# Optimization experiments

Hardware: AMD Instinct MI355X
Metric: run time of the kernel (lower is better)

## Reference

```python
import jax, jax.numpy as jnp
import numpy as np


def setup_inputs() -> dict:
    key = jax.random.key(0)
    ks = jax.random.split(key, 5)
    B, T, D, E = 4, 2048, 1024, 8
    inputs = jax.random.normal(ks[0], (B, T, D), dtype=jnp.float32)
    Wr = jax.random.normal(ks[1], (D, E), dtype=jnp.float32) * 0.02
    br = jnp.zeros((E,), dtype=jnp.float32)
    W1 = jax.random.normal(ks[2], (E, D, D), dtype=jnp.float32) * 0.02
    b1 = jnp.zeros((E, D), dtype=jnp.float32)
    W2 = jax.random.normal(ks[3], (E, D, D), dtype=jnp.float32) * 0.02
    b2 = jnp.zeros((E, D), dtype=jnp.float32)
    return {"inputs": inputs, "Wr": Wr, "br": br, "W1": W1, "b1": b1, "W2": W2, "b2": b2}


def reference(inputs, Wr, br, W1, b1, W2, b2):
    B, T, D = inputs.shape
    E = Wr.shape[1]
    x = inputs.reshape(B * T, D)            # [N, D]
    N = x.shape[0]
    C = N // E                              # expert capacity

    # --- Router (top-1), inference path (no training noise) ---
    logits = x @ Wr + br                    # [N, E]
    probs = jax.nn.softmax(logits, axis=-1)
    gate = jnp.max(probs, axis=-1, keepdims=True)     # [N, 1] expert_gate
    idx = jnp.argmax(probs, axis=-1)                  # [N]
    mask = jax.nn.one_hot(idx, E, dtype=jnp.float32)  # [N, E]

    # 1-based position of each token within its chosen expert (0 elsewhere)
    pos = (jnp.cumsum(mask, axis=0) * mask).astype(jnp.int32)  # [N, E]
    # capacity check uses the 1-based position (faithful to original)
    mask = mask * (pos < C).astype(jnp.float32)
    mask_flat = jnp.sum(mask, axis=-1, keepdims=True)          # [N, 1]
    gate = gate * mask_flat                                    # [N, 1]

    # combine tensor [N, E, C]; slots for non-chosen experts (pos==0 -> one_hot slot 0)
    # are zeroed by the gate*one_hot(idx) factor, as in the original.
    combine = (gate * mask_flat * jax.nn.one_hot(idx, E, dtype=jnp.float32))[..., None] \
              * jax.nn.one_hot(pos, C, dtype=jnp.float32)      # [N, E, C]
    dispatch = combine                                         # float32 cast is identity

    # --- Dispatch: dense einsum (faithful to original anti-pattern) ---
    expert_in = jnp.einsum('nd,nec->ecd', x, dispatch)         # [E, C, D]

    # --- Per-expert FFN as grouped GEMM: Dense(D, relu) -> Dense(D) ---
    h = jax.nn.relu(jnp.einsum('ecd,edf->ecf', expert_in, W1) + b1[:, None, :])
    eo = jnp.einsum('ecf,efd->ecd', h, W2) + b2[:, None, :]    # [E, C, D]

    # --- Combine ---
    out = jnp.einsum('ecd,nec->nd', eo, combine)               # [N, D]
    return out.reshape(B, T, D)
```

## Files before the change

kernel.cpp:

```cpp
#include <hip/hip_runtime.h>
#include <hip/hip_bf16.h>
#include <stdint.h>

#define N_TOK 8192
#define DIM   1024
#define NEXP  8
#define CAP   1024

typedef __attribute__((ext_vector_type(8))) short bf16x8;
typedef __attribute__((ext_vector_type(4))) float f32x4;

static __device__ __forceinline__ unsigned short f2bf(float f) {
  unsigned int u = __float_as_uint(f);
  u += 0x7FFFu + ((u >> 16) & 1u);
  return (unsigned short)(u >> 16);
}

static __device__ __forceinline__ void gld_lds16(const void* g, void* l) {
  __builtin_amdgcn_global_load_lds(
      (__attribute__((address_space(1))) void*)(uintptr_t)g,
      (__attribute__((address_space(3))) void*)(unsigned int)(uintptr_t)l,
      16, 0, 0);
}

__global__ void router_kernel(const float* __restrict__ x, const float* __restrict__ Wr,
                              const float* __restrict__ br, float* __restrict__ gate,
                              int* __restrict__ idxs) {
  const int wid  = (blockIdx.x * blockDim.x + threadIdx.x) >> 6;
  const int lane = threadIdx.x & 63;
  const float* xr = x + (size_t)wid * DIM;
  double acc[8] = {0,0,0,0,0,0,0,0};
  #pragma unroll 4
  for (int j = 0; j < 16; ++j) {
    const int d = j * 64 + lane;
    const double xv = (double)xr[d];
    const float4 wa = *(const float4*)(Wr + d * 8);
    const float4 wb = *(const float4*)(Wr + d * 8 + 4);
    acc[0] += xv * (double)wa.x;  acc[1] += xv * (double)wa.y;
    acc[2] += xv * (double)wa.z;  acc[3] += xv * (double)wa.w;
    acc[4] += xv * (double)wb.x;  acc[5] += xv * (double)wb.y;
    acc[6] += xv * (double)wb.z;  acc[7] += xv * (double)wb.w;
  }
  #pragma unroll
  for (int off = 1; off < 64; off <<= 1) {
    #pragma unroll
    for (int e = 0; e < 8; ++e) acc[e] += __shfl_xor(acc[e], off);
  }
  if (lane == 0) {
    double lg[8];
    #pragma unroll
    for (int e = 0; e < 8; ++e) lg[e] = acc[e] + (double)br[e];
    int best = 0; double bm = lg[0];
    #pragma unroll
    for (int e = 1; e < 8; ++e) { if (lg[e] > bm) { bm = lg[e]; best = e; } }
    double s = 0.0;
    #pragma unroll
    for (int e = 0; e < 8; ++e) s += exp(lg[e] - bm);
    gate[wid] = (float)(1.0 / s);
    idxs[wid] = best;
  }
}

__global__ void scan_kernel(const int* __restrict__ idxs, int* __restrict__ slot_token,
                            int* __restrict__ keep) {
  __shared__ int wtot[16][8];
  const int t = threadIdx.x, lane = t & 63, w = t >> 6;
  #pragma unroll
  for (int j = 0; j < 8; ++j) slot_token[t * 8 + j] = -1;
  int myidx[8];
  #pragma unroll
  for (int j = 0; j < 8; ++j) myidx[j] = idxs[t * 8 + j];
  int cnt[8], incl[8];
  #pragma unroll
  for (int e = 0; e < 8; ++e) {
    int c = 0;
    #pragma unroll
    for (int j = 0; j < 8; ++j) c += (myidx[j] == e) ? 1 : 0;
    cnt[e] = c;
    int v = c;
    #pragma unroll
    for (int off = 1; off < 64; off <<= 1) {
      int u = __shfl_up(v, off);
      if (lane >= off) v += u;
    }
    incl[e] = v;
  }
  if (lane == 63) {
    #pragma unroll
    for (int e = 0; e < 8; ++e) wtot[w][e] = incl[e];
  }
  __syncthreads();
  if (t == 0) {
    int run[8] = {0,0,0,0,0,0,0,0};
    for (int ww = 0; ww < 16; ++ww) {
      #pragma unroll
      for (int e = 0; e < 8; ++e) {
        int tmp = wtot[ww][e]; wtot[ww][e] = run[e]; run[e] += tmp;
      }
    }
  }
  __syncthreads();
  #pragma unroll
  for (int e = 0; e < 8; ++e) {
    int r = wtot[w][e] + incl[e] - cnt[e];
    #pragma unroll
    for (int j = 0; j < 8; ++j) {
      if (myidx[j] == e) {
        ++r;
        const int kept = (r < CAP) ? 1 : 0;
        keep[t * 8 + j] = kept;
        if (kept) slot_token[e * CAP + r] = t * 8 + j;
      }
    }
  }
}

__global__ void util_kernel(const float* __restrict__ W1, const float* __restrict__ W2,
                            unsigned short* __restrict__ W1T, unsigned short* __restrict__ W2T,
                            const float* __restrict__ x, const float* __restrict__ gate,
                            const int* __restrict__ slot_token, const int* __restrict__ keep,
                            unsigned short* __restrict__ Xe, float* __restrict__ out) {
  const int t = threadIdx.x;
  if (blockIdx.x < 16384) {
    __shared__ float tile[32][33];
    const int mi = blockIdx.x >> 10;
    const int tz = blockIdx.x & 1023;
    const int tr = tz >> 5, tc = tz & 31;
    const float* src = (mi < 8) ? (W1 + (size_t)mi * DIM * DIM)
                                : (W2 + (size_t)(mi - 8) * DIM * DIM);
    unsigned short* dst = (mi < 8) ? (W1T + (size_t)mi * DIM * DIM)
                                   : (W2T + (size_t)(mi - 8) * DIM * DIM);
    const int row = t >> 3;
    const int cg  = (t & 7) * 4;
    const float4 v = *(const float4*)(src + (size_t)(tr * 32 + row) * DIM + tc * 32 + cg);
    tile[row][cg + 0] = v.x; tile[row][cg + 1] = v.y;
    tile[row][cg + 2] = v.z; tile[row][cg + 3] = v.w;
    __syncthreads();
    ushort4 o;
    o.x = f2bf(tile[cg + 0][row]); o.y = f2bf(tile[cg + 1][row]);
    o.z = f2bf(tile[cg + 2][row]); o.w = f2bf(tile[cg + 3][row]);
    *(ushort4*)(dst + (size_t)(tc * 32 + row) * DIM + tr * 32 + cg) = o;
  } else if (blockIdx.x < 16384 + NEXP * CAP) {
    const int s = blockIdx.x - 16384;
    const int n = slot_token[s];
    if (n < 0) return;
    const float g = gate[n];
    const float4 v = ((const float4*)(x + (size_t)n * DIM))[t];
    ushort4 o;
    o.x = f2bf(v.x * g); o.y = f2bf(v.y * g); o.z = f2bf(v.z * g); o.w = f2bf(v.w * g);
    ((ushort4*)(Xe + (size_t)s * DIM))[t] = o;
  } else {
    const int n = blockIdx.x - (16384 + NEXP * CAP);
    if (keep[n]) return;
    float4 z = {0.f, 0.f, 0.f, 0.f};
    ((float4*)(out + (size_t)n * DIM))[t] = z;
  }
}

template <int OP>
__global__ __launch_bounds__(256)
void gemm_kernel(const unsigned short* __restrict__ A,
                 const unsigned short* __restrict__ Bt,
                 const float* __restrict__ bias,
                 const int* __restrict__ slot_token,
                 const float* __restrict__ gate,
                 unsigned short* __restrict__ Hout,
                 float* __restrict__ Cout)
{
  __shared__ unsigned short Asub[3][128 * 32];
  __shared__ unsigned short Bsub[3][128 * 32];
  const int bid = blockIdx.x;
  const int e  = bid & 7;
  const int tt = bid >> 3;
  const int bm = tt >> 3;
  const int bn = tt & 7;
  const int tid = threadIdx.x, lane = tid & 63, w = tid >> 6;
  const int wr = w >> 1, wc = w & 1;

  const unsigned short* Ae = A  + (size_t)(e * CAP + bm * 128) * DIM;
  const unsigned short* Be = Bt + (size_t)e * DIM * DIM + (size_t)(bn * 128) * DIM;

  const int srow = lane >> 2;
  const int scol = (((lane & 3) ^ ((lane >> 3) & 3)) * 8);
  const int lrow = lane & 15;
  const int kof  = (((lane >> 4) ^ ((lrow >> 1) & 3)) * 8);

  f32x4 acc[4][4] = {};

  auto stage = [&](int buf, int kt) {
    const int k0 = kt * 32;
    #pragma unroll
    for (int c = 0; c < 2; ++c) {
      const int chunk = w + c * 4;
      const int r = chunk * 16 + srow;
      gld_lds16(Ae + (size_t)r * DIM + k0 + scol, &Asub[buf][chunk * 512]);
      gld_lds16(Be + (size_t)r * DIM + k0 + scol, &Bsub[buf][chunk * 512]);
    }
  };
  auto compute = [&](int buf) {
    bf16x8 af[4], bfr[4];
    #pragma unroll
    for (int m = 0; m < 4; ++m)
      af[m] = *(const bf16x8*)&Asub[buf][(wr * 64 + m * 16 + lrow) * 32 + kof];
    #pragma unroll
    for (int n = 0; n < 4; ++n)
      bfr[n] = *(const bf16x8*)&Bsub[buf][(wc * 64 + n * 16 + lrow) * 32 + kof];
    #pragma unroll
    for (int m = 0; m < 4; ++m)
      #pragma unroll
      for (int n = 0; n < 4; ++n)
        acc[m][n] = __builtin_amdgcn_mfma_f32_16x16x32_bf16(af[m], bfr[n], acc[m][n], 0, 0, 0);
  };

  stage(0, 0);
  stage(1, 1);
  asm volatile("s_waitcnt vmcnt(4)" ::: "memory");
  __builtin_amdgcn_s_barrier();
  int b0 = 0, b1 = 1, b2 = 2;
  for (int kt = 0; kt < 32; ++kt) {
    if (kt < 30) stage(b2, kt + 2);
    compute(b0);
    if (kt == 31) break;
    if (kt < 30) asm volatile("s_waitcnt vmcnt(4)" ::: "memory");
    else         asm volatile("s_waitcnt vmcnt(0)" ::: "memory");
    __builtin_amdgcn_s_barrier();
    const int tb = b0; b0 = b1; b1 = b2; b2 = tb;
  }

  if (OP == 1) {
    #pragma unroll
    for (int n = 0; n < 4; ++n) {
      const int col = bn * 128 + wc * 64 + n * 16 + lrow;
      const float bv = bias[e * DIM + col];
      #pragma unroll
      for (int m = 0; m < 4; ++m) {
        const int r0 = bm * 128 + wr * 64 + m * 16 + (lane >> 4) * 4;
        #pragma unroll
        for (int i = 0; i < 4; ++i) {
          float v = acc[m][n][i] + bv;
          v = v > 0.0f ? v : 0.0f;
          Hout[(size_t)(e * CAP + r0 + i) * DIM + col] = f2bf(v);
        }
      }
    }
  } else {
    float bv[4];
    #pragma unroll
    for (int n = 0; n < 4; ++n)
      bv[n] = bias[e * DIM + bn * 128 + wc * 64 + n * 16 + lrow];
    #pragma unroll
    for (int m = 0; m < 4; ++m) {
      const int r0 = bm * 128 + wr * 64 + m * 16 + (lane >> 4) * 4;
      #pragma unroll
      for (int i = 0; i < 4; ++i) {
        const int tok = slot_token[e * CAP + r0 + i];
        if (tok >= 0) {
          const float g = gate[tok];
          float* orow = Cout + (size_t)tok * DIM;
          #pragma unroll
          for (int n = 0; n < 4; ++n) {
            const int col = bn * 128 + wc * 64 + n * 16 + lrow;
            orow[col] = g * (acc[m][n][i] + bv[n]);
          }
        }
      }
    }
  }
}

extern "C" void kernel_launch(void* const* d_in, const int* in_sizes, int n_in,
                              void* d_out, int out_size, void* d_ws, size_t ws_size,
                              hipStream_t stream) {
  const float* x  = (const float*)d_in[0];
  const float* Wr = (const float*)d_in[1];
  const float* br = (const float*)d_in[2];
  const float* W1 = (const float*)d_in[3];
  const float* b1 = (const float*)d_in[4];
  const float* W2 = (const float*)d_in[5];
  const float* b2 = (const float*)d_in[6];
  float* out = (float*)d_out;

  char* ws = (char*)d_ws;
  unsigned short* Xe  = (unsigned short*)(ws);
  unsigned short* Hh  = (unsigned short*)(ws + (size_t)16 * 1024 * 1024);
  unsigned short* W1T = (unsigned short*)(ws + (size_t)32 * 1024 * 1024);
  unsigned short* W2T = (unsigned short*)(ws + (size_t)48 * 1024 * 1024);
  float* gate     = (float*)(ws + (size_t)64 * 1024 * 1024);
  int*   idxs     = (int*)  (ws + (size_t)64 * 1024 * 1024 + 32768);
  int*   slot_tok = (int*)  (ws + (size_t)64 * 1024 * 1024 + 65536);
  int*   keep     = (int*)  (ws + (size_t)64 * 1024 * 1024 + 98304);

  router_kernel<<<2048, 256, 0, stream>>>(x, Wr, br, gate, idxs);
  scan_kernel<<<1, 1024, 0, stream>>>(idxs, slot_tok, keep);
  util_kernel<<<32768, 256, 0, stream>>>(W1, W2, W1T, W2T, x, gate, slot_tok, keep, Xe, out);
  gemm_kernel<1><<<512, 256, 0, stream>>>(Xe, W1T, b1, nullptr, nullptr, Hh, nullptr);
  gemm_kernel<2><<<512, 256, 0, stream>>>(Hh, W2T, b2, slot_tok, gate, nullptr, out);
}
```

Baseline: 236.5 us.

## Fuse router with scan and both expert GEMMs, widen transpose tiles

```diff
diff --git a/kernel.cpp b/kernel.cpp
--- a/kernel.cpp
+++ b/kernel.cpp
@@ -23,61 +23,71 @@
       16, 0, 0);
 }
 
-__global__ void router_kernel(const float* __restrict__ x, const float* __restrict__ Wr,
-                              const float* __restrict__ br, float* __restrict__ gate,
-                              int* __restrict__ idxs) {
-  const int wid  = (blockIdx.x * blockDim.x + threadIdx.x) >> 6;
-  const int lane = threadIdx.x & 63;
-  const float* xr = x + (size_t)wid * DIM;
-  double acc[8] = {0,0,0,0,0,0,0,0};
-  #pragma unroll 4
-  for (int j = 0; j < 16; ++j) {
-    const int d = j * 64 + lane;
-    const double xv = (double)xr[d];
-    const float4 wa = *(const float4*)(Wr + d * 8);
-    const float4 wb = *(const float4*)(Wr + d * 8 + 4);
-    acc[0] += xv * (double)wa.x;  acc[1] += xv * (double)wa.y;
-    acc[2] += xv * (double)wa.z;  acc[3] += xv * (double)wa.w;
-    acc[4] += xv * (double)wb.x;  acc[5] += xv * (double)wb.y;
-    acc[6] += xv * (double)wb.z;  acc[7] += xv * (double)wb.w;
-  }
+__global__ __launch_bounds__(256)
+void router_scan_kernel(const float* __restrict__ x, const float* __restrict__ Wr,
+                        const float* __restrict__ br, float* __restrict__ gate,
+                        int* __restrict__ idxs, int* __restrict__ slot_token,
+                        int* __restrict__ keep, unsigned int* __restrict__ rs_ctr) {
+  const int t = threadIdx.x, lane = t & 63, w = t >> 6;
+  const int tok = blockIdx.x * 4 + w;
+  {
+    const float* xr = x + (size_t)tok * DIM;
+    double acc[8] = {0,0,0,0,0,0,0,0};
+    #pragma unroll 4
+    for (int j = 0; j < 16; ++j) {
+      const int d = j * 64 + lane;
+      const double xv = (double)xr[d];
+      const float4 wa = *(const float4*)(Wr + d * 8);
+      const float4 wb = *(const float4*)(Wr + d * 8 + 4);
+      acc[0] += xv * (double)wa.x;  acc[1] += xv * (double)wa.y;
+      acc[2] += xv * (double)wa.z;  acc[3] += xv * (double)wa.w;
+      acc[4] += xv * (double)wb.x;  acc[5] += xv * (double)wb.y;
+      acc[6] += xv * (double)wb.z;  acc[7] += xv * (double)wb.w;
+    }
+    #pragma unroll
+    for (int off = 1; off < 64; off <<= 1) {
+      #pragma unroll
+      for (int e = 0; e < 8; ++e) acc[e] += __shfl_xor(acc[e], off);
+    }
+    if (lane == 0) {
+      double lg[8];
+      #pragma unroll
+      for (int e = 0; e < 8; ++e) lg[e] = acc[e] + (double)br[e];
+      int best = 0; double bm = lg[0];
+      #pragma unroll
+      for (int e = 1; e < 8; ++e) { if (lg[e] > bm) { bm = lg[e]; best = e; } }
+      double s = 0.0;
+      #pragma unroll
+      for (int e = 0; e < 8; ++e) s += exp(lg[e] - bm);
+      gate[tok] = (float)(1.0 / s);
+      idxs[tok] = best;
+    }
+  }
+
+  __shared__ int is_last;
+  __syncthreads();
+  if (t == 0) {
+    __threadfence();
+    unsigned int old = atomicAdd(rs_ctr, 1u);
+    is_last = (old == 2047u) ? 1 : 0;
+  }
+  __syncthreads();
+  if (!is_last) return;
+  __threadfence();
+
+  __shared__ int wtot[4][8];
+  __shared__ int rbuf[256][8];
+  for (int j = t; j < NEXP * CAP; j += 256) slot_token[j] = -1;
+  __syncthreads();
+  const int base = t * 32;
   #pragma unroll
-  for (int off = 1; off < 64; off <<= 1) {
-    #pragma unroll
-    for (int e = 0; e < 8; ++e) acc[e] += __shfl_xor(acc[e], off);
-  }
-  if (lane == 0) {
-    double lg[8];
-    #pragma unroll
-    for (int e = 0; e < 8; ++e) lg[e] = acc[e] + (double)br[e];
-    int best = 0; double bm = lg[0];
-    #pragma unroll
-    for (int e = 1; e < 8; ++e) { if (lg[e] > bm) { bm = lg[e]; best = e; } }
-    double s = 0.0;
-    #pragma unroll
-    for (int e = 0; e < 8; ++e) s += exp(lg[e] - bm);
-    gate[wid] = (float)(1.0 / s);
-    idxs[wid] = best;
-  }
-}
-
-__global__ void scan_kernel(const int* __restrict__ idxs, int* __restrict__ slot_token,
-                            int* __restrict__ keep) {
-  __shared__ int wtot[16][8];
-  const int t = threadIdx.x, lane = t & 63, w = t >> 6;
-  #pragma unroll
-  for (int j = 0; j < 8; ++j) slot_token[t * 8 + j] = -1;
-  int myidx[8];
-  #pragma unroll
-  for (int j = 0; j < 8; ++j) myidx[j] = idxs[t * 8 + j];
+  for (int e = 0; e < 8; ++e) rbuf[t][e] = 0;
+  for (int j = 0; j < 32; ++j) rbuf[t][idxs[base + j]] += 1;
   int cnt[8], incl[8];
   #pragma unroll
   for (int e = 0; e < 8; ++e) {
-    int c = 0;
-    #pragma unroll
-    for (int j = 0; j < 8; ++j) c += (myidx[j] == e) ? 1 : 0;
-    cnt[e] = c;
-    int v = c;
+    cnt[e] = rbuf[t][e];
+    int v = cnt[e];
     #pragma unroll
     for (int off = 1; off < 64; off <<= 1) {
       int u = __shfl_up(v, off);
@@ -92,56 +102,60 @@
   __syncthreads();
   if (t == 0) {
     int run[8] = {0,0,0,0,0,0,0,0};
-    for (int ww = 0; ww < 16; ++ww) {
-      #pragma unroll
-      for (int e = 0; e < 8; ++e) {
-        int tmp = wtot[ww][e]; wtot[ww][e] = run[e]; run[e] += tmp;
-      }
+    for (int ww = 0; ww < 4; ++ww) {
+      #pragma unroll
+      for (int e = 0; e < 8; ++e) { int tmp = wtot[ww][e]; wtot[ww][e] = run[e]; run[e] += tmp; }
     }
   }
   __syncthreads();
   #pragma unroll
-  for (int e = 0; e < 8; ++e) {
-    int r = wtot[w][e] + incl[e] - cnt[e];
-    #pragma unroll
-    for (int j = 0; j < 8; ++j) {
-      if (myidx[j] == e) {
-        ++r;
-        const int kept = (r < CAP) ? 1 : 0;
-        keep[t * 8 + j] = kept;
-        if (kept) slot_token[e * CAP + r] = t * 8 + j;
-      }
-    }
-  }
-}
-
-__global__ void util_kernel(const float* __restrict__ W1, const float* __restrict__ W2,
-                            unsigned short* __restrict__ W1T, unsigned short* __restrict__ W2T,
-                            const float* __restrict__ x, const float* __restrict__ gate,
-                            const int* __restrict__ slot_token, const int* __restrict__ keep,
-                            unsigned short* __restrict__ Xe, float* __restrict__ out) {
+  for (int e = 0; e < 8; ++e) rbuf[t][e] = wtot[w][e] + incl[e] - cnt[e];
+  for (int j = 0; j < 32; ++j) {
+    const int n = base + j;
+    const int e = idxs[n];
+    const int r = ++rbuf[t][e];
+    const int kept = (r < CAP) ? 1 : 0;
+    keep[n] = kept;
+    if (kept) slot_token[e * CAP + r] = n;
+  }
+}
+
+__global__ __launch_bounds__(256)
+void util_kernel(const float* __restrict__ W1, const float* __restrict__ W2,
+                 unsigned short* __restrict__ W1T, unsigned short* __restrict__ W2T,
+                 const float* __restrict__ x, const float* __restrict__ gate,
+                 const int* __restrict__ slot_token, const int* __restrict__ keep,
+                 unsigned short* __restrict__ Xe, float* __restrict__ out) {
   const int t = threadIdx.x;
-  if (blockIdx.x < 16384) {
-    __shared__ float tile[32][33];
-    const int mi = blockIdx.x >> 10;
-    const int tz = blockIdx.x & 1023;
-    const int tr = tz >> 5, tc = tz & 31;
+  if (blockIdx.x < 4096) {
+    __shared__ float tile[64][65];
+    const int mi = blockIdx.x >> 8;
+    const int tz = blockIdx.x & 255;
+    const int tr = tz >> 4, tc = tz & 15;
     const float* src = (mi < 8) ? (W1 + (size_t)mi * DIM * DIM)
                                 : (W2 + (size_t)(mi - 8) * DIM * DIM);
     unsigned short* dst = (mi < 8) ? (W1T + (size_t)mi * DIM * DIM)
                                    : (W2T + (size_t)(mi - 8) * DIM * DIM);
-    const int row = t >> 3;
-    const int cg  = (t & 7) * 4;
-    const float4 v = *(const float4*)(src + (size_t)(tr * 32 + row) * DIM + tc * 32 + cg);
-    tile[row][cg + 0] = v.x; tile[row][cg + 1] = v.y;
-    tile[row][cg + 2] = v.z; tile[row][cg + 3] = v.w;
+    #pragma unroll
+    for (int q = 0; q < 4; ++q) {
+      const int row = q * 16 + (t >> 4);
+      const int c4  = (t & 15) * 4;
+      const float4 v = *(const float4*)(src + (size_t)(tr * 64 + row) * DIM + tc * 64 + c4);
+      tile[row][c4 + 0] = v.x; tile[row][c4 + 1] = v.y;
+      tile[row][c4 + 2] = v.z; tile[row][c4 + 3] = v.w;
+    }
     __syncthreads();
-    ushort4 o;
-    o.x = f2bf(tile[cg + 0][row]); o.y = f2bf(tile[cg + 1][row]);
-    o.z = f2bf(tile[cg + 2][row]); o.w = f2bf(tile[cg + 3][row]);
-    *(ushort4*)(dst + (size_t)(tc * 32 + row) * DIM + tr * 32 + cg) = o;
-  } else if (blockIdx.x < 16384 + NEXP * CAP) {
-    const int s = blockIdx.x - 16384;
+    #pragma unroll
+    for (int p = 0; p < 2; ++p) {
+      const int n  = p * 32 + (t >> 3);
+      const int k0 = (t & 7) * 8;
+      bf16x8 o;
+      #pragma unroll
+      for (int j = 0; j < 8; ++j) o[j] = (short)f2bf(tile[k0 + j][n]);
+      *(bf16x8*)(dst + (size_t)(tc * 64 + n) * DIM + tr * 64 + k0) = o;
+    }
+  } else if (blockIdx.x < 4096 + NEXP * CAP) {
+    const int s = blockIdx.x - 4096;
     const int n = slot_token[s];
     if (n < 0) return;
     const float g = gate[n];
@@ -150,7 +164,7 @@
     o.x = f2bf(v.x * g); o.y = f2bf(v.y * g); o.z = f2bf(v.z * g); o.w = f2bf(v.w * g);
     ((ushort4*)(Xe + (size_t)s * DIM))[t] = o;
   } else {
-    const int n = blockIdx.x - (16384 + NEXP * CAP);
+    const int n = blockIdx.x - (4096 + NEXP * CAP);
     if (keep[n]) return;
     float4 z = {0.f, 0.f, 0.f, 0.f};
     ((float4*)(out + (size_t)n * DIM))[t] = z;
@@ -158,17 +172,12 @@
 }
 
 template <int OP>
-__global__ __launch_bounds__(256)
-void gemm_kernel(const unsigned short* __restrict__ A,
-                 const unsigned short* __restrict__ Bt,
-                 const float* __restrict__ bias,
-                 const int* __restrict__ slot_token,
-                 const float* __restrict__ gate,
-                 unsigned short* __restrict__ Hout,
-                 float* __restrict__ Cout)
-{
-  __shared__ unsigned short Asub[3][128 * 32];
-  __shared__ unsigned short Bsub[3][128 * 32];
+static __device__ __forceinline__ void gemm_body(
+    unsigned short* Asub, unsigned short* Bsub,
+    const unsigned short* __restrict__ A, const unsigned short* __restrict__ Bt,
+    const float* __restrict__ bias, const int* __restrict__ slot_token,
+    const float* __restrict__ gate, unsigned short* __restrict__ Hout,
+    float* __restrict__ Cout) {
   const int bid = blockIdx.x;
   const int e  = bid & 7;
   const int tt = bid >> 3;
@@ -193,18 +202,18 @@
     for (int c = 0; c < 2; ++c) {
       const int chunk = w + c * 4;
       const int r = chunk * 16 + srow;
-      gld_lds16(Ae + (size_t)r * DIM + k0 + scol, &Asub[buf][chunk * 512]);
-      gld_lds16(Be + (size_t)r * DIM + k0 + scol, &Bsub[buf][chunk * 512]);
+      gld_lds16(Ae + (size_t)r * DIM + k0 + scol, &Asub[buf * 4096 + chunk * 512]);
+      gld_lds16(Be + (size_t)r * DIM + k0 + scol, &Bsub[buf * 4096 + chunk * 512]);
     }
   };
   auto compute = [&](int buf) {
     bf16x8 af[4], bfr[4];
     #pragma unroll
     for (int m = 0; m < 4; ++m)
-      af[m] = *(const bf16x8*)&Asub[buf][(wr * 64 + m * 16 + lrow) * 32 + kof];
+      af[m] = *(const bf16x8*)&Asub[buf * 4096 + (wr * 64 + m * 16 + lrow) * 32 + kof];
     #pragma unroll
     for (int n = 0; n < 4; ++n)
-      bfr[n] = *(const bf16x8*)&Bsub[buf][(wc * 64 + n * 16 + lrow) * 32 + kof];
+      bfr[n] = *(const bf16x8*)&Bsub[buf * 4096 + (wc * 64 + n * 16 + lrow) * 32 + kof];
     #pragma unroll
     for (int m = 0; m < 4; ++m)
       #pragma unroll
@@ -228,19 +237,30 @@
   }
 
   if (OP == 1) {
-    #pragma unroll
-    for (int n = 0; n < 4; ++n) {
-      const int col = bn * 128 + wc * 64 + n * 16 + lrow;
-      const float bv = bias[e * DIM + col];
-      #pragma unroll
-      for (int m = 0; m < 4; ++m) {
-        const int r0 = bm * 128 + wr * 64 + m * 16 + (lane >> 4) * 4;
+    unsigned short* slab = Asub;
+    #pragma unroll
+    for (int m = 0; m < 4; ++m) {
+      __syncthreads();
+      #pragma unroll
+      for (int n = 0; n < 4; ++n) {
+        const int col = wc * 64 + n * 16 + lrow;
+        const float bv = bias[e * DIM + bn * 128 + col];
         #pragma unroll
         for (int i = 0; i < 4; ++i) {
+          const int lr = wr * 16 + (lane >> 4) * 4 + i;
           float v = acc[m][n][i] + bv;
           v = v > 0.0f ? v : 0.0f;
-          Hout[(size_t)(e * CAP + r0 + i) * DIM + col] = f2bf(v);
+          slab[lr * 128 + col] = f2bf(v);
         }
+      }
+      __syncthreads();
+      #pragma unroll
+      for (int p = 0; p < 2; ++p) {
+        const int lr = (tid >> 4) + p * 16;
+        const int c0 = (tid & 15) * 8;
+        const int grow = bm * 128 + (lr >> 4) * 64 + m * 16 + (lr & 15);
+        *(bf16x8*)(Hout + (size_t)(e * CAP + grow) * DIM + bn * 128 + c0) =
+            *(const bf16x8*)&slab[lr * 128 + c0];
       }
     }
   } else {
@@ -268,6 +288,36 @@
   }
 }
 
+__global__ __launch_bounds__(256)
+void moe_gemm_kernel(const unsigned short* __restrict__ Xe,
+                     const unsigned short* __restrict__ W1T, const float* __restrict__ b1,
+                     const unsigned short* __restrict__ W2T, const float* __restrict__ b2,
+                     unsigned short* __restrict__ Hh, float* __restrict__ out,
+                     const int* __restrict__ slot_token, const float* __restrict__ gate,
+                     unsigned int* __restrict__ panel_ctr) {
+  __shared__ unsigned short Asub[3 * 4096];
+  __shared__ unsigned short Bsub[3 * 4096];
+  const int e  = blockIdx.x & 7;
+  const int bm = (blockIdx.x >> 3) >> 3;
+  const int tid = threadIdx.x;
+
+  gemm_body<1>(Asub, Bsub, Xe, W1T, b1, nullptr, nullptr, Hh, nullptr);
+
+  __shared__ int ready;
+  __syncthreads();
+  __threadfence();
+  if (tid == 0) {
+    atomicAdd(&panel_ctr[e * 8 + bm], 1u);
+    while (atomicAdd(&panel_ctr[e * 8 + bm], 0u) < 8u) { __builtin_amdgcn_s_sleep(8); }
+    ready = 1;
+  }
+  __syncthreads();
+  (void)ready;
+  __threadfence();
+
+  gemm_body<2>(Asub, Bsub, Hh, W2T, b2, slot_token, gate, nullptr, out);
+}
+
 extern "C" void kernel_launch(void* const* d_in, const int* in_sizes, int n_in,
                               void* d_out, int out_size, void* d_ws, size_t ws_size,
                               hipStream_t stream) {
@@ -289,10 +339,13 @@
   int*   idxs     = (int*)  (ws + (size_t)64 * 1024 * 1024 + 32768);
   int*   slot_tok = (int*)  (ws + (size_t)64 * 1024 * 1024 + 65536);
   int*   keep     = (int*)  (ws + (size_t)64 * 1024 * 1024 + 98304);
-
-  router_kernel<<<2048, 256, 0, stream>>>(x, Wr, br, gate, idxs);
-  scan_kernel<<<1, 1024, 0, stream>>>(idxs, slot_tok, keep);
-  util_kernel<<<32768, 256, 0, stream>>>(W1, W2, W1T, W2T, x, gate, slot_tok, keep, Xe, out);
-  gemm_kernel<1><<<512, 256, 0, stream>>>(Xe, W1T, b1, nullptr, nullptr, Hh, nullptr);
-  gemm_kernel<2><<<512, 256, 0, stream>>>(Hh, W2T, b2, slot_tok, gate, nullptr, out);
-}
+  unsigned int* ctrs = (unsigned int*)(ws + (size_t)64 * 1024 * 1024 + 131072);
+  unsigned int* rs_ctr    = ctrs;
+  unsigned int* panel_ctr = ctrs + 16;
+
+  hipMemsetAsync(ctrs, 0, 512, stream);
+  router_scan_kernel<<<2048, 256, 0, stream>>>(x, Wr, br, gate, idxs, slot_tok, keep, rs_ctr);
+  util_kernel<<<20480, 256, 0, stream>>>(W1, W2, W1T, W2T, x, gate, slot_tok, keep, Xe, out);
+  moe_gemm_kernel<<<512, 256, 0, stream>>>(Xe, W1T, b1, W2T, b2, Hh, out, slot_tok, gate,
+                                           panel_ctr);
+}
```

Measured after the change: 406.9 us. +72.1%, slower.
